# Optimization experiments

Hardware: AMD Instinct MI355X
Metric: run time of the kernel (lower is better)

Reference implementation:

```python
import jax, jax.numpy as jnp
import numpy as np
import math

# Dims chosen per input_specs
B, Q, S, T = 8, 64, 64, 64          # batch, queries, stat (segment) count, tokens per segment
H, DH = 8, 64                        # heads, head dim
NH = H * DH                          # num_hiddens = 512
STAT_K, TOKEN_K = 8, 16
NEG = -1e6


def setup_inputs() -> dict:
    key = jax.random.key(0)
    ks = jax.random.split(key, 11)
    f = lambda k, sh: jax.random.normal(k, sh, dtype=jnp.float32)
    w = lambda k: f(k, (NH, NH)) * 0.05  # Linear weights stored as [in, out]
    return {
        "queries": f(ks[0], (B, Q, NH)),
        "stat_keys": f(ks[1], (B, S, NH)),
        "token_keys": f(ks[2], (B * S, T, NH)),
        "values": f(ks[3], (B * S, T, NH)),
        "stat_valid_lens": jax.random.randint(ks[4], (B,), 1, S + 1, dtype=jnp.int32),
        "Wq_stat": w(ks[5]),
        "Wq_token": w(ks[6]),
        "Wk_stat": w(ks[7]),
        "Wk_token": w(ks[8]),
        "Wv": w(ks[9]),
        "Wo": w(ks[10]),
    }


def reference(queries, stat_keys, token_keys, values, stat_valid_lens,
              Wq_stat, Wq_token, Wk_stat, Wk_token, Wv, Wo):
    scale = 1.0 / math.sqrt(DH)

    def split_heads(x):  # [b, L, H*DH] -> [b, H, L, DH]
        b, L, _ = x.shape
        return x.reshape(b, L, H, DH).transpose(0, 2, 1, 3)

    q_stat = split_heads(queries @ Wq_stat)        # [B,H,Q,DH]
    q_tok = split_heads(queries @ Wq_token)        # [B,H,Q,DH]
    k_stat = split_heads(stat_keys @ Wk_stat)      # [B,H,S,DH]
    # token_keys/values come in as [B*S, T, size]; per-head layout [B,H,S,T,DH]
    k_tok = (token_keys @ Wk_token).reshape(B, S, T, H, DH).transpose(0, 3, 1, 2, 4)
    v = (values @ Wv).reshape(B, S, T, H, DH).transpose(0, 3, 1, 2, 4)

    # --- stat-level scores, valid-length mask, top-k sparsification, softmax ---
    stat_scores = jnp.einsum('bhqd,bhsd->bhqs', q_stat, k_stat) * scale  # [B,H,Q,S]
    valid = jnp.arange(S)[None, None, None, :] < stat_valid_lens[:, None, None, None]
    stat_scores = jnp.where(valid, stat_scores, NEG)
    k1 = min(S - 1, STAT_K)
    _, top_idx = jax.lax.top_k(stat_scores, k1)                           # [B,H,Q,k1]
    keep = jax.nn.one_hot(top_idx, S, dtype=stat_scores.dtype).sum(-2) > 0  # [B,H,Q,S]
    stat_w = jax.nn.softmax(jnp.where(keep, stat_scores, NEG), axis=-1)   # [B,H,Q,S]

    # --- token-level scores. NOTE: the original code computes torch.topk but then
    # overwrites with the LAST k2 positions (token_weights[:, :, -k2:] = ...), so the
    # token top-k result is dead code; we faithfully reproduce the last-k2 masking. ---
    tok_scores = jnp.einsum('bhqd,bhstd->bhsqt', q_tok, k_tok) * scale    # [B,H,S,Q,T]
    k2 = min(T - 1, TOKEN_K)
    last_mask = jnp.arange(T) >= (T - k2)
    tok_w = jax.nn.softmax(jnp.where(last_mask, tok_scores, NEG), axis=-1)
    tok_w = tok_w.transpose(0, 1, 3, 2, 4)                                # [B,H,Q,S,T]

    # --- combine hierarchy and attend over values ---
    comb = stat_w[..., None] * tok_w                                      # [B,H,Q,S,T]
    out = jnp.einsum('bhqst,bhstd->bhqd', comb, v)                        # [B,H,Q,DH]
    out = out.transpose(0, 2, 1, 3).reshape(B, Q, NH)
    return out @ Wo
```

## Files before the change

kernel.cpp:

```cpp
#include <hip/hip_runtime.h>
#include <hip/hip_bf16.h>

#define BB 8
#define QQ 64
#define SS 64
#define TT 64
#define HH 8
#define DH 64
#define NHID 512
#define STAT_K 8
#define TOKEN_K 16

typedef short bf16x8 __attribute__((ext_vector_type(8)));
typedef float f32x4 __attribute__((ext_vector_type(4)));

__device__ inline ushort f2bf_rne(float x) {
    union { float f; unsigned u; } v; v.f = x;
    unsigned r = v.u + 0x7fff + ((v.u >> 16) & 1);
    return (ushort)(r >> 16);
}
__device__ inline float bf2f(ushort h) {
    union { unsigned u; float f; } v; v.u = ((unsigned)h) << 16;
    return v.f;
}

__global__ __launch_bounds__(256) void conv_all(
    const float* w0, const float* w1, const float* w2,
    const float* w3, const float* w4, const float* w5,
    const float* queries, const float* stat_keys,
    ushort* wT, ushort* q_hi, ushort* q_lo, ushort* sk_hi, ushort* sk_lo)
{
    const int z = blockIdx.z;
    if (z < 6) {
        const float* srcs[6] = {w0, w1, w2, w3, w4, w5};
        const float* src = srcs[z];
        ushort* hi = wT + (size_t)z * 524288;
        ushort* lo = hi + 262144;
        __shared__ float t[32][33];
        const int c0 = blockIdx.x * 32, r0 = blockIdx.y * 32;
        const int tx = threadIdx.x & 31, ty = threadIdx.x >> 5;
        #pragma unroll
        for (int i = 0; i < 4; ++i)
            t[ty + 8 * i][tx] = src[(r0 + ty + 8 * i) * 512 + c0 + tx];
        __syncthreads();
        #pragma unroll
        for (int i = 0; i < 4; ++i) {
            float x = t[tx][ty + 8 * i];
            ushort h = f2bf_rne(x);
            int o = (c0 + ty + 8 * i) * 512 + r0 + tx;
            hi[o] = h;
            lo[o] = f2bf_rne(x - bf2f(h));
        }
    } else {
        const float* src = (z == 6) ? queries : stat_keys;
        ushort* hi = (z == 6) ? q_hi : sk_hi;
        ushort* lo = (z == 6) ? q_lo : sk_lo;
        int base = (blockIdx.y * 16 + blockIdx.x) * 1024 + threadIdx.x * 4;
        float4 x = *(const float4*)(src + base);
        ushort4 h, l;
        h.x = f2bf_rne(x.x); l.x = f2bf_rne(x.x - bf2f(h.x));
        h.y = f2bf_rne(x.y); l.y = f2bf_rne(x.y - bf2f(h.y));
        h.z = f2bf_rne(x.z); l.z = f2bf_rne(x.z - bf2f(h.z));
        h.w = f2bf_rne(x.w); l.w = f2bf_rne(x.w - bf2f(h.w));
        *(ushort4*)(hi + base) = h;
        *(ushort4*)(lo + base) = l;
    }
}

__global__ __launch_bounds__(256) void gemm_split3(
    const ushort* __restrict__ q_hi, const ushort* __restrict__ q_lo,
    const ushort* __restrict__ sk_hi, const ushort* __restrict__ sk_lo,
    const ushort* __restrict__ wT,
    float* __restrict__ q_stat, float* __restrict__ k_stat,
    float* __restrict__ q_tokf)
{
    const int z = blockIdx.z;
    const ushort* Ah = (z == 1) ? sk_hi : q_hi;
    const ushort* Al = (z == 1) ? sk_lo : q_lo;
    const ushort* Bh = wT + (size_t)z * 524288;
    const ushort* Bl = Bh + 262144;
    float* C = (z == 0) ? q_stat : (z == 1) ? k_stat : q_tokf;
    const int K = 512, N = 512;

    __shared__ ushort As[2][64][40];
    __shared__ ushort Bs[2][64][40];
    const int tid = threadIdx.x;
    const int row0 = blockIdx.y * 64, col0 = blockIdx.x * 64;
    const int wave = tid >> 6, lane = tid & 63;
    const int wm = wave & 1, wn = wave >> 1;
    const int m16 = lane & 15, quad = lane >> 4;
    const int srow = tid >> 2, schunk = tid & 3;

    f32x4 acc[2][2];
    #pragma unroll
    for (int i = 0; i < 2; ++i)
        #pragma unroll
        for (int j = 0; j < 2; ++j)
            #pragma unroll
            for (int r = 0; r < 4; ++r) acc[i][j][r] = 0.f;

    for (int k0 = 0; k0 < K; k0 += 32) {
        const size_t aoff = (size_t)(row0 + srow) * K + k0 + schunk * 8;
        const size_t boff = (size_t)(col0 + srow) * K + k0 + schunk * 8;
        *(uint4*)&As[0][srow][schunk * 8] = *(const uint4*)(Ah + aoff);
        *(uint4*)&Bs[0][srow][schunk * 8] = *(const uint4*)(Bh + boff);
        *(uint4*)&As[1][srow][schunk * 8] = *(const uint4*)(Al + aoff);
        *(uint4*)&Bs[1][srow][schunk * 8] = *(const uint4*)(Bl + boff);
        __syncthreads();

        bf16x8 af[2], bf[2], afl[2], bfl[2];
        #pragma unroll
        for (int i = 0; i < 2; ++i) {
            af[i]  = *(const bf16x8*)&As[0][wm * 32 + i * 16 + m16][quad * 8];
            bf[i]  = *(const bf16x8*)&Bs[0][wn * 32 + i * 16 + m16][quad * 8];
            afl[i] = *(const bf16x8*)&As[1][wm * 32 + i * 16 + m16][quad * 8];
            bfl[i] = *(const bf16x8*)&Bs[1][wn * 32 + i * 16 + m16][quad * 8];
        }
        #pragma unroll
        for (int i = 0; i < 2; ++i)
            #pragma unroll
            for (int j = 0; j < 2; ++j) {
                acc[i][j] = __builtin_amdgcn_mfma_f32_16x16x32_bf16(af[i], bf[j], acc[i][j], 0, 0, 0);
                acc[i][j] = __builtin_amdgcn_mfma_f32_16x16x32_bf16(af[i], bfl[j], acc[i][j], 0, 0, 0);
                acc[i][j] = __builtin_amdgcn_mfma_f32_16x16x32_bf16(afl[i], bf[j], acc[i][j], 0, 0, 0);
            }
        __syncthreads();
    }

    #pragma unroll
    for (int i = 0; i < 2; ++i)
        #pragma unroll
        for (int j = 0; j < 2; ++j) {
            int r0 = row0 + wm * 32 + i * 16 + quad * 4;
            int c = col0 + wn * 32 + j * 16 + m16;
            #pragma unroll
            for (int reg = 0; reg < 4; ++reg)
                C[(size_t)(r0 + reg) * N + c] = acc[i][j][reg];
        }
}

__global__ __launch_bounds__(256) void gemm_out(
    const ushort* __restrict__ Ah, const ushort* __restrict__ Al,
    const ushort* __restrict__ Bh, const ushort* __restrict__ Bl,
    float* __restrict__ C)
{
    const int K = 512, N = 512;
    __shared__ ushort As[2][64][40];
    __shared__ ushort Bs[2][64][40];
    const int tid = threadIdx.x;
    const int row0 = blockIdx.y * 64, col0 = blockIdx.x * 64;
    const int wave = tid >> 6, lane = tid & 63;
    const int wm = wave & 1, wn = wave >> 1;
    const int m16 = lane & 15, quad = lane >> 4;
    const int srow = tid >> 2, schunk = tid & 3;

    f32x4 acc[2][2];
    #pragma unroll
    for (int i = 0; i < 2; ++i)
        #pragma unroll
        for (int j = 0; j < 2; ++j)
            #pragma unroll
            for (int r = 0; r < 4; ++r) acc[i][j][r] = 0.f;

    for (int k0 = 0; k0 < K; k0 += 32) {
        const size_t aoff = (size_t)(row0 + srow) * K + k0 + schunk * 8;
        const size_t boff = (size_t)(col0 + srow) * K + k0 + schunk * 8;
        *(uint4*)&As[0][srow][schunk * 8] = *(const uint4*)(Ah + aoff);
        *(uint4*)&Bs[0][srow][schunk * 8] = *(const uint4*)(Bh + boff);
        *(uint4*)&As[1][srow][schunk * 8] = *(const uint4*)(Al + aoff);
        *(uint4*)&Bs[1][srow][schunk * 8] = *(const uint4*)(Bl + boff);
        __syncthreads();

        bf16x8 af[2], bf[2], afl[2], bfl[2];
        #pragma unroll
        for (int i = 0; i < 2; ++i) {
            af[i]  = *(const bf16x8*)&As[0][wm * 32 + i * 16 + m16][quad * 8];
            bf[i]  = *(const bf16x8*)&Bs[0][wn * 32 + i * 16 + m16][quad * 8];
            afl[i] = *(const bf16x8*)&As[1][wm * 32 + i * 16 + m16][quad * 8];
            bfl[i] = *(const bf16x8*)&Bs[1][wn * 32 + i * 16 + m16][quad * 8];
        }
        #pragma unroll
        for (int i = 0; i < 2; ++i)
            #pragma unroll
            for (int j = 0; j < 2; ++j) {
                acc[i][j] = __builtin_amdgcn_mfma_f32_16x16x32_bf16(af[i], bf[j], acc[i][j], 0, 0, 0);
                acc[i][j] = __builtin_amdgcn_mfma_f32_16x16x32_bf16(af[i], bfl[j], acc[i][j], 0, 0, 0);
                acc[i][j] = __builtin_amdgcn_mfma_f32_16x16x32_bf16(afl[i], bf[j], acc[i][j], 0, 0, 0);
            }
        __syncthreads();
    }

    #pragma unroll
    for (int i = 0; i < 2; ++i)
        #pragma unroll
        for (int j = 0; j < 2; ++j) {
            int r0 = row0 + wm * 32 + i * 16 + quad * 4;
            int c = col0 + wn * 32 + j * 16 + m16;
            #pragma unroll
            for (int reg = 0; reg < 4; ++reg)
                C[(size_t)(r0 + reg) * N + c] = acc[i][j][reg];
        }
}

__global__ __launch_bounds__(256) void gemm_tok(
    const float* __restrict__ token_keys, const float* __restrict__ values,
    const ushort* __restrict__ wkt_h, const ushort* __restrict__ wv_h,
    ushort* __restrict__ k_tok, ushort* __restrict__ v_proj)
{
    const int z = blockIdx.z;
    const float* A = z ? values : token_keys;
    const ushort* Bh = z ? wv_h : wkt_h;
    ushort* C = z ? v_proj : k_tok;
    const int K = 512, N = 512;

    __shared__ ushort As[64][40];
    __shared__ ushort Bs[256][40];
    const int tid = threadIdx.x;
    const int row0 = blockIdx.y * 64, col0 = blockIdx.x * 256;
    const int wave = tid >> 6, lane = tid & 63;
    const int m16 = lane & 15, quad = lane >> 4;
    const int srow = tid >> 2, schunk = tid & 3;

    const int r = row0 + srow;
    const size_t arow = (size_t)((r >> 4) * 64 + 48 + (r & 15)) * K;

    f32x4 acc[4][4];
    #pragma unroll
    for (int i = 0; i < 4; ++i)
        #pragma unroll
        for (int j = 0; j < 4; ++j)
            #pragma unroll
            for (int rr = 0; rr < 4; ++rr) acc[i][j][rr] = 0.f;

    for (int k0 = 0; k0 < K; k0 += 32) {
        const float* ap = A + arow + k0 + schunk * 8;
        float4 x0 = ((const float4*)ap)[0];
        float4 x1 = ((const float4*)ap)[1];
        ushort4 h0, h1;
        h0.x = f2bf_rne(x0.x); h0.y = f2bf_rne(x0.y);
        h0.z = f2bf_rne(x0.z); h0.w = f2bf_rne(x0.w);
        h1.x = f2bf_rne(x1.x); h1.y = f2bf_rne(x1.y);
        h1.z = f2bf_rne(x1.z); h1.w = f2bf_rne(x1.w);
        *(ushort4*)&As[srow][schunk * 8] = h0;
        *(ushort4*)&As[srow][schunk * 8 + 4] = h1;
        #pragma unroll
        for (int i = 0; i < 4; ++i) {
            int v = tid + i * 256;
            int brow = v >> 2, bchunk = v & 3;
            *(uint4*)&Bs[brow][bchunk * 8] =
                *(const uint4*)(Bh + (size_t)(col0 + brow) * K + k0 + bchunk * 8);
        }
        __syncthreads();

        bf16x8 af[4], bf[4];
        #pragma unroll
        for (int i = 0; i < 4; ++i) {
            af[i] = *(const bf16x8*)&As[i * 16 + m16][quad * 8];
            bf[i] = *(const bf16x8*)&Bs[wave * 64 + i * 16 + m16][quad * 8];
        }
        #pragma unroll
        for (int i = 0; i < 4; ++i)
            #pragma unroll
            for (int j = 0; j < 4; ++j)
                acc[i][j] = __builtin_amdgcn_mfma_f32_16x16x32_bf16(af[i], bf[j], acc[i][j], 0, 0, 0);
        __syncthreads();
    }

    #pragma unroll
    for (int i = 0; i < 4; ++i)
        #pragma unroll
        for (int j = 0; j < 4; ++j) {
            int r0 = row0 + i * 16 + quad * 4;
            int c = col0 + wave * 64 + j * 16 + m16;
            #pragma unroll
            for (int reg = 0; reg < 4; ++reg)
                C[(size_t)(r0 + reg) * N + c] = f2bf_rne(acc[i][j][reg]);
        }
}

__global__ __launch_bounds__(64) void stat_topk(
    const float* __restrict__ q_stat, const float* __restrict__ k_stat,
    const int* __restrict__ valid_lens,
    int* __restrict__ sel_idx, float* __restrict__ sel_w)
{
    const int bid = blockIdx.x;
    const int b = bid >> 9;
    const int hq = bid & 511;
    const int h = hq >> 6;
    const int q = hq & 63;
    const int lane = threadIdx.x;

    __shared__ float sq[64];
    sq[lane] = q_stat[(b * QQ + q) * NHID + h * DH + lane];
    __syncthreads();

    const float4* kr = (const float4*)(k_stat + (b * SS + lane) * NHID + h * DH);
    const float4* sq4 = (const float4*)sq;
    float sc = 0.f;
    #pragma unroll
    for (int i = 0; i < 16; ++i) {
        float4 a = sq4[i], kk = kr[i];
        sc += a.x * kk.x + a.y * kk.y + a.z * kk.z + a.w * kk.w;
    }
    sc *= 0.125f;
    if (lane >= valid_lens[b]) sc = -1e6f;

    float my = sc;
    float mv[STAT_K];
    int   mi[STAT_K];
    #pragma unroll
    for (int j = 0; j < STAT_K; ++j) {
        float v = my;
        int idx = lane;
        #pragma unroll
        for (int off = 32; off > 0; off >>= 1) {
            float ov = __shfl_down(v, off);
            int   oi = __shfl_down(idx, off);
            if (ov > v || (ov == v && oi < idx)) { v = ov; idx = oi; }
        }
        v = __shfl(v, 0);
        idx = __shfl(idx, 0);
        mv[j] = v; mi[j] = idx;
        if (lane == idx) my = -3e38f;
    }
    float m0 = mv[0];
    float den = 0.f;
    float w[STAT_K];
    #pragma unroll
    for (int j = 0; j < STAT_K; ++j) { w[j] = __expf(mv[j] - m0); den += w[j]; }
    float inv = 1.f / den;
    if (lane < STAT_K) {
        sel_idx[bid * STAT_K + lane] = mi[lane];
        sel_w[bid * STAT_K + lane]   = w[lane] * inv;
    }
}

__global__ __launch_bounds__(64) void token_attend2(
    const float* __restrict__ q_tok, const ushort* __restrict__ k_tok,
    const ushort* __restrict__ v_proj, const int* __restrict__ sel_idx,
    const float* __restrict__ sel_w,
    ushort* __restrict__ ctx_hi, ushort* __restrict__ ctx_lo)
{
    const int bid = blockIdx.x;
    const int b = bid >> 9, h = (bid >> 6) & 7, q = bid & 63;
    const int lane = threadIdx.x;

    __shared__ float sq[64];
    __shared__ float ssc[16];
    __shared__ int   ssel[STAT_K];
    __shared__ float ssw[STAT_K];

    sq[lane] = q_tok[(size_t)(b * QQ + q) * NHID + h * DH + lane];
    if (lane < STAT_K) {
        ssel[lane] = sel_idx[bid * STAT_K + lane];
        ssw[lane]  = sel_w[bid * STAT_K + lane];
    }
    __syncthreads();

    const int t = lane >> 2, part = lane & 3;
    float acc = 0.f;

    for (int j = 0; j < STAT_K; ++j) {
        const int s = ssel[j];
        const float wseg = ssw[j];
        const size_t rowbase = (size_t)((b * SS + s) * TOKEN_K);

        const uint4* k4 = (const uint4*)(k_tok + (rowbase + t) * NHID + h * DH + part * 16);
        uint4 ka = k4[0], kb = k4[1];
        const float* qb = &sq[part * 16];
        float p = 0.f;
        p += qb[0]  * bf2f((ushort)(ka.x & 0xffff)) + qb[1]  * bf2f((ushort)(ka.x >> 16));
        p += qb[2]  * bf2f((ushort)(ka.y & 0xffff)) + qb[3]  * bf2f((ushort)(ka.y >> 16));
        p += qb[4]  * bf2f((ushort)(ka.z & 0xffff)) + qb[5]  * bf2f((ushort)(ka.z >> 16));
        p += qb[6]  * bf2f((ushort)(ka.w & 0xffff)) + qb[7]  * bf2f((ushort)(ka.w >> 16));
        p += qb[8]  * bf2f((ushort)(kb.x & 0xffff)) + qb[9]  * bf2f((ushort)(kb.x >> 16));
        p += qb[10] * bf2f((ushort)(kb.y & 0xffff)) + qb[11] * bf2f((ushort)(kb.y >> 16));
        p += qb[12] * bf2f((ushort)(kb.z & 0xffff)) + qb[13] * bf2f((ushort)(kb.z >> 16));
        p += qb[14] * bf2f((ushort)(kb.w & 0xffff)) + qb[15] * bf2f((ushort)(kb.w >> 16));
        p += __shfl_xor(p, 1);
        p += __shfl_xor(p, 2);
        if (part == 0) ssc[t] = p * 0.125f;
        __syncthreads();

        float m = ssc[0];
        #pragma unroll
        for (int tt = 1; tt < TOKEN_K; ++tt) m = fmaxf(m, ssc[tt]);
        float den = 0.f, wv[TOKEN_K];
        #pragma unroll
        for (int tt = 0; tt < TOKEN_K; ++tt) { wv[tt] = __expf(ssc[tt] - m); den += wv[tt]; }

        const ushort* vrow = v_proj + rowbase * NHID + h * DH + lane;
        float loc = 0.f;
        #pragma unroll
        for (int tt = 0; tt < TOKEN_K; ++tt) loc += wv[tt] * bf2f(vrow[tt * NHID]);
        acc += (wseg / den) * loc;
        __syncthreads();
    }

    const size_t o = (size_t)(b * QQ + q) * NHID + h * DH + lane;
    ushort hh = f2bf_rne(acc);
    ctx_hi[o] = hh;
    ctx_lo[o] = f2bf_rne(acc - bf2f(hh));
}

extern "C" void kernel_launch(void* const* d_in, const int* in_sizes, int n_in,
                              void* d_out, int out_size, void* d_ws, size_t ws_size,
                              hipStream_t stream) {
    const float* queries    = (const float*)d_in[0];
    const float* stat_keys  = (const float*)d_in[1];
    const float* token_keys = (const float*)d_in[2];
    const float* values     = (const float*)d_in[3];
    const int*   valid_lens = (const int*)d_in[4];
    const float* Wq_stat    = (const float*)d_in[5];
    const float* Wq_token   = (const float*)d_in[6];
    const float* Wk_stat    = (const float*)d_in[7];
    const float* Wk_token   = (const float*)d_in[8];
    const float* Wv         = (const float*)d_in[9];
    const float* Wo         = (const float*)d_in[10];

    char* w = (char*)d_ws;
    ushort* wT      = (ushort*)(w + 0);
    ushort* q_hi    = (ushort*)(w + 6291456);
    ushort* q_lo    = q_hi + 262144;
    ushort* sk_hi   = (ushort*)(w + 7340032);
    ushort* sk_lo   = sk_hi + 262144;
    float*  q_stat  = (float*)(w + 8388608);
    float*  k_stat  = (float*)(w + 9437184);
    float*  q_tokf  = (float*)(w + 10485760);
    ushort* k_tok   = (ushort*)(w + 11534336);
    ushort* v_projp = (ushort*)(w + 19922944);
    ushort* ctx_hi  = (ushort*)(w + 28311552);
    ushort* ctx_lo  = ctx_hi + 262144;
    float*  sel_w   = (float*)(w + 29360128);
    int*    sel_idx = (int*)(w + 29491200);

    ushort* wkt_h = wT + 3 * 524288;
    ushort* wv_h  = wT + 4 * 524288;
    ushort* wo_h  = wT + 5 * 524288, *wo_l = wo_h + 262144;

    conv_all<<<dim3(16, 16, 8), 256, 0, stream>>>(
        Wq_stat, Wk_stat, Wq_token, Wk_token, Wv, Wo,
        queries, stat_keys, wT, q_hi, q_lo, sk_hi, sk_lo);

    gemm_split3<<<dim3(8, 8, 3), 256, 0, stream>>>(
        q_hi, q_lo, sk_hi, sk_lo, wT, q_stat, k_stat, q_tokf);

    stat_topk<<<4096, 64, 0, stream>>>(q_stat, k_stat, valid_lens, sel_idx, sel_w);

    gemm_tok<<<dim3(2, 128, 2), 256, 0, stream>>>(
        token_keys, values, wkt_h, wv_h, k_tok, v_projp);

    token_attend2<<<4096, 64, 0, stream>>>(q_tokf, k_tok, v_projp,
                                           sel_idx, sel_w, ctx_hi, ctx_lo);

    gemm_out<<<dim3(8, 8), 256, 0, stream>>>(
        ctx_hi, ctx_lo, wo_h, wo_l, (float*)d_out);
}
```

Before: 224.4 us.

## Fuse stat top-k into token attend, convert inputs inside GEMM, register-prefetch tiles

Merges the stat-score top-k kernel into the token attention kernel, so selected indices and weights stay in registers and one launch plus a global round trip are removed. The hi/lo bf16 split of queries and stat keys moves into the projection GEMM's tile load, which drops those workspace buffers and part of the conversion kernel. All three GEMMs now prefetch the next K tile into registers while the current tile is computed. The prefetch raises register pressure, and the fused attention kernel does more serial work per block.

```diff
diff --git a/kernel.cpp b/kernel.cpp
--- a/kernel.cpp
+++ b/kernel.cpp
@@ -24,59 +24,40 @@
     return v.f;
 }
 
-__global__ __launch_bounds__(256) void conv_all(
+__global__ __launch_bounds__(256) void conv_w(
     const float* w0, const float* w1, const float* w2,
-    const float* w3, const float* w4, const float* w5,
-    const float* queries, const float* stat_keys,
-    ushort* wT, ushort* q_hi, ushort* q_lo, ushort* sk_hi, ushort* sk_lo)
+    const float* w3, const float* w4, const float* w5, ushort* wT)
 {
     const int z = blockIdx.z;
-    if (z < 6) {
-        const float* srcs[6] = {w0, w1, w2, w3, w4, w5};
-        const float* src = srcs[z];
-        ushort* hi = wT + (size_t)z * 524288;
-        ushort* lo = hi + 262144;
-        __shared__ float t[32][33];
-        const int c0 = blockIdx.x * 32, r0 = blockIdx.y * 32;
-        const int tx = threadIdx.x & 31, ty = threadIdx.x >> 5;
-        #pragma unroll
-        for (int i = 0; i < 4; ++i)
-            t[ty + 8 * i][tx] = src[(r0 + ty + 8 * i) * 512 + c0 + tx];
-        __syncthreads();
-        #pragma unroll
-        for (int i = 0; i < 4; ++i) {
-            float x = t[tx][ty + 8 * i];
-            ushort h = f2bf_rne(x);
-            int o = (c0 + ty + 8 * i) * 512 + r0 + tx;
-            hi[o] = h;
-            lo[o] = f2bf_rne(x - bf2f(h));
-        }
-    } else {
-        const float* src = (z == 6) ? queries : stat_keys;
-        ushort* hi = (z == 6) ? q_hi : sk_hi;
-        ushort* lo = (z == 6) ? q_lo : sk_lo;
-        int base = (blockIdx.y * 16 + blockIdx.x) * 1024 + threadIdx.x * 4;
-        float4 x = *(const float4*)(src + base);
-        ushort4 h, l;
-        h.x = f2bf_rne(x.x); l.x = f2bf_rne(x.x - bf2f(h.x));
-        h.y = f2bf_rne(x.y); l.y = f2bf_rne(x.y - bf2f(h.y));
-        h.z = f2bf_rne(x.z); l.z = f2bf_rne(x.z - bf2f(h.z));
-        h.w = f2bf_rne(x.w); l.w = f2bf_rne(x.w - bf2f(h.w));
-        *(ushort4*)(hi + base) = h;
-        *(ushort4*)(lo + base) = l;
+    const float* srcs[6] = {w0, w1, w2, w3, w4, w5};
+    const float* src = srcs[z];
+    ushort* hi = wT + (size_t)z * 524288;
+    ushort* lo = hi + 262144;
+    __shared__ float t[32][33];
+    const int c0 = blockIdx.x * 32, r0 = blockIdx.y * 32;
+    const int tx = threadIdx.x & 31, ty = threadIdx.x >> 5;
+    #pragma unroll
+    for (int i = 0; i < 4; ++i)
+        t[ty + 8 * i][tx] = src[(r0 + ty + 8 * i) * 512 + c0 + tx];
+    __syncthreads();
+    #pragma unroll
+    for (int i = 0; i < 4; ++i) {
+        float x = t[tx][ty + 8 * i];
+        ushort h = f2bf_rne(x);
+        int o = (c0 + ty + 8 * i) * 512 + r0 + tx;
+        hi[o] = h;
+        lo[o] = f2bf_rne(x - bf2f(h));
     }
 }
 
 __global__ __launch_bounds__(256) void gemm_split3(
-    const ushort* __restrict__ q_hi, const ushort* __restrict__ q_lo,
-    const ushort* __restrict__ sk_hi, const ushort* __restrict__ sk_lo,
+    const float* __restrict__ queries, const float* __restrict__ stat_keys,
     const ushort* __restrict__ wT,
     float* __restrict__ q_stat, float* __restrict__ k_stat,
     float* __restrict__ q_tokf)
 {
     const int z = blockIdx.z;
-    const ushort* Ah = (z == 1) ? sk_hi : q_hi;
-    const ushort* Al = (z == 1) ? sk_lo : q_lo;
+    const float* Afp = (z == 1) ? stat_keys : queries;
     const ushort* Bh = wT + (size_t)z * 524288;
     const ushort* Bl = Bh + 262144;
     float* C = (z == 0) ? q_stat : (z == 1) ? k_stat : q_tokf;
@@ -91,6 +72,15 @@
     const int m16 = lane & 15, quad = lane >> 4;
     const int srow = tid >> 2, schunk = tid & 3;
 
+    const float*  aptr  = Afp + (size_t)(row0 + srow) * K + schunk * 8;
+    const ushort* bptrh = Bh + (size_t)(col0 + srow) * K + schunk * 8;
+    const ushort* bptrl = Bl + (size_t)(col0 + srow) * K + schunk * 8;
+
+    float4 ax0 = ((const float4*)aptr)[0];
+    float4 ax1 = ((const float4*)aptr)[1];
+    uint4  bvh = *(const uint4*)bptrh;
+    uint4  bvl = *(const uint4*)bptrl;
+
     f32x4 acc[2][2];
     #pragma unroll
     for (int i = 0; i < 2; ++i)
@@ -100,13 +90,29 @@
             for (int r = 0; r < 4; ++r) acc[i][j][r] = 0.f;
 
     for (int k0 = 0; k0 < K; k0 += 32) {
-        const size_t aoff = (size_t)(row0 + srow) * K + k0 + schunk * 8;
-        const size_t boff = (size_t)(col0 + srow) * K + k0 + schunk * 8;
-        *(uint4*)&As[0][srow][schunk * 8] = *(const uint4*)(Ah + aoff);
-        *(uint4*)&Bs[0][srow][schunk * 8] = *(const uint4*)(Bh + boff);
-        *(uint4*)&As[1][srow][schunk * 8] = *(const uint4*)(Al + aoff);
-        *(uint4*)&Bs[1][srow][schunk * 8] = *(const uint4*)(Bl + boff);
-        __syncthreads();
+        ushort4 h0, h1, l0, l1;
+        h0.x = f2bf_rne(ax0.x); l0.x = f2bf_rne(ax0.x - bf2f(h0.x));
+        h0.y = f2bf_rne(ax0.y); l0.y = f2bf_rne(ax0.y - bf2f(h0.y));
+        h0.z = f2bf_rne(ax0.z); l0.z = f2bf_rne(ax0.z - bf2f(h0.z));
+        h0.w = f2bf_rne(ax0.w); l0.w = f2bf_rne(ax0.w - bf2f(h0.w));
+        h1.x = f2bf_rne(ax1.x); l1.x = f2bf_rne(ax1.x - bf2f(h1.x));
+        h1.y = f2bf_rne(ax1.y); l1.y = f2bf_rne(ax1.y - bf2f(h1.y));
+        h1.z = f2bf_rne(ax1.z); l1.z = f2bf_rne(ax1.z - bf2f(h1.z));
+        h1.w = f2bf_rne(ax1.w); l1.w = f2bf_rne(ax1.w - bf2f(h1.w));
+        *(ushort4*)&As[0][srow][schunk * 8]     = h0;
+        *(ushort4*)&As[0][srow][schunk * 8 + 4] = h1;
+        *(ushort4*)&As[1][srow][schunk * 8]     = l0;
+        *(ushort4*)&As[1][srow][schunk * 8 + 4] = l1;
+        *(uint4*)&Bs[0][srow][schunk * 8] = bvh;
+        *(uint4*)&Bs[1][srow][schunk * 8] = bvl;
+        __syncthreads();
+
+        if (k0 + 32 < K) {
+            ax0 = ((const float4*)(aptr + k0 + 32))[0];
+            ax1 = ((const float4*)(aptr + k0 + 32))[1];
+            bvh = *(const uint4*)(bptrh + k0 + 32);
+            bvl = *(const uint4*)(bptrl + k0 + 32);
+        }
 
         bf16x8 af[2], bf[2], afl[2], bfl[2];
         #pragma unroll
@@ -154,6 +160,16 @@
     const int m16 = lane & 15, quad = lane >> 4;
     const int srow = tid >> 2, schunk = tid & 3;
 
+    const ushort* aptrh = Ah + (size_t)(row0 + srow) * K + schunk * 8;
+    const ushort* aptrl = Al + (size_t)(row0 + srow) * K + schunk * 8;
+    const ushort* bptrh = Bh + (size_t)(col0 + srow) * K + schunk * 8;
+    const ushort* bptrl = Bl + (size_t)(col0 + srow) * K + schunk * 8;
+
+    uint4 avh = *(const uint4*)aptrh;
+    uint4 avl = *(const uint4*)aptrl;
+    uint4 bvh = *(const uint4*)bptrh;
+    uint4 bvl = *(const uint4*)bptrl;
+
     f32x4 acc[2][2];
     #pragma unroll
     for (int i = 0; i < 2; ++i)
@@ -163,13 +179,18 @@
             for (int r = 0; r < 4; ++r) acc[i][j][r] = 0.f;
 
     for (int k0 = 0; k0 < K; k0 += 32) {
-        const size_t aoff = (size_t)(row0 + srow) * K + k0 + schunk * 8;
-        const size_t boff = (size_t)(col0 + srow) * K + k0 + schunk * 8;
-        *(uint4*)&As[0][srow][schunk * 8] = *(const uint4*)(Ah + aoff);
-        *(uint4*)&Bs[0][srow][schunk * 8] = *(const uint4*)(Bh + boff);
-        *(uint4*)&As[1][srow][schunk * 8] = *(const uint4*)(Al + aoff);
-        *(uint4*)&Bs[1][srow][schunk * 8] = *(const uint4*)(Bl + boff);
-        __syncthreads();
+        *(uint4*)&As[0][srow][schunk * 8] = avh;
+        *(uint4*)&As[1][srow][schunk * 8] = avl;
+        *(uint4*)&Bs[0][srow][schunk * 8] = bvh;
+        *(uint4*)&Bs[1][srow][schunk * 8] = bvl;
+        __syncthreads();
+
+        if (k0 + 32 < K) {
+            avh = *(const uint4*)(aptrh + k0 + 32);
+            avl = *(const uint4*)(aptrl + k0 + 32);
+            bvh = *(const uint4*)(bptrh + k0 + 32);
+            bvl = *(const uint4*)(bptrl + k0 + 32);
+        }
 
         bf16x8 af[2], bf[2], afl[2], bfl[2];
         #pragma unroll
@@ -222,7 +243,16 @@
     const int srow = tid >> 2, schunk = tid & 3;
 
     const int r = row0 + srow;
-    const size_t arow = (size_t)((r >> 4) * 64 + 48 + (r & 15)) * K;
+    const float* aptr = A + (size_t)((r >> 4) * 64 + 48 + (r & 15)) * K + schunk * 8;
+
+    float4 ax0 = ((const float4*)aptr)[0];
+    float4 ax1 = ((const float4*)aptr)[1];
+    uint4 bv[4];
+    #pragma unroll
+    for (int i = 0; i < 4; ++i) {
+        int v = tid + i * 256;
+        bv[i] = *(const uint4*)(Bh + (size_t)(col0 + (v >> 2)) * K + (v & 3) * 8);
+    }
 
     f32x4 acc[4][4];
     #pragma unroll
@@ -233,24 +263,29 @@
             for (int rr = 0; rr < 4; ++rr) acc[i][j][rr] = 0.f;
 
     for (int k0 = 0; k0 < K; k0 += 32) {
-        const float* ap = A + arow + k0 + schunk * 8;
-        float4 x0 = ((const float4*)ap)[0];
-        float4 x1 = ((const float4*)ap)[1];
         ushort4 h0, h1;
-        h0.x = f2bf_rne(x0.x); h0.y = f2bf_rne(x0.y);
-        h0.z = f2bf_rne(x0.z); h0.w = f2bf_rne(x0.w);
-        h1.x = f2bf_rne(x1.x); h1.y = f2bf_rne(x1.y);
-        h1.z = f2bf_rne(x1.z); h1.w = f2bf_rne(x1.w);
-        *(ushort4*)&As[srow][schunk * 8] = h0;
+        h0.x = f2bf_rne(ax0.x); h0.y = f2bf_rne(ax0.y);
+        h0.z = f2bf_rne(ax0.z); h0.w = f2bf_rne(ax0.w);
+        h1.x = f2bf_rne(ax1.x); h1.y = f2bf_rne(ax1.y);
+        h1.z = f2bf_rne(ax1.z); h1.w = f2bf_rne(ax1.w);
+        *(ushort4*)&As[srow][schunk * 8]     = h0;
         *(ushort4*)&As[srow][schunk * 8 + 4] = h1;
         #pragma unroll
         for (int i = 0; i < 4; ++i) {
             int v = tid + i * 256;
-            int brow = v >> 2, bchunk = v & 3;
-            *(uint4*)&Bs[brow][bchunk * 8] =
-                *(const uint4*)(Bh + (size_t)(col0 + brow) * K + k0 + bchunk * 8);
-        }
-        __syncthreads();
+            *(uint4*)&Bs[v >> 2][(v & 3) * 8] = bv[i];
+        }
+        __syncthreads();
+
+        if (k0 + 32 < K) {
+            ax0 = ((const float4*)(aptr + k0 + 32))[0];
+            ax1 = ((const float4*)(aptr + k0 + 32))[1];
+            #pragma unroll
+            for (int i = 0; i < 4; ++i) {
+                int v = tid + i * 256;
+                bv[i] = *(const uint4*)(Bh + (size_t)(col0 + (v >> 2)) * K + (v & 3) * 8 + k0 + 32);
+            }
+        }
 
         bf16x8 af[4], bf[4];
         #pragma unroll
@@ -278,67 +313,10 @@
         }
 }
 
-__global__ __launch_bounds__(64) void stat_topk(
+__global__ __launch_bounds__(64) void attend_fused(
     const float* __restrict__ q_stat, const float* __restrict__ k_stat,
-    const int* __restrict__ valid_lens,
-    int* __restrict__ sel_idx, float* __restrict__ sel_w)
-{
-    const int bid = blockIdx.x;
-    const int b = bid >> 9;
-    const int hq = bid & 511;
-    const int h = hq >> 6;
-    const int q = hq & 63;
-    const int lane = threadIdx.x;
-
-    __shared__ float sq[64];
-    sq[lane] = q_stat[(b * QQ + q) * NHID + h * DH + lane];
-    __syncthreads();
-
-    const float4* kr = (const float4*)(k_stat + (b * SS + lane) * NHID + h * DH);
-    const float4* sq4 = (const float4*)sq;
-    float sc = 0.f;
-    #pragma unroll
-    for (int i = 0; i < 16; ++i) {
-        float4 a = sq4[i], kk = kr[i];
-        sc += a.x * kk.x + a.y * kk.y + a.z * kk.z + a.w * kk.w;
-    }
-    sc *= 0.125f;
-    if (lane >= valid_lens[b]) sc = -1e6f;
-
-    float my = sc;
-    float mv[STAT_K];
-    int   mi[STAT_K];
-    #pragma unroll
-    for (int j = 0; j < STAT_K; ++j) {
-        float v = my;
-        int idx = lane;
-        #pragma unroll
-        for (int off = 32; off > 0; off >>= 1) {
-            float ov = __shfl_down(v, off);
-            int   oi = __shfl_down(idx, off);
-            if (ov > v || (ov == v && oi < idx)) { v = ov; idx = oi; }
-        }
-        v = __shfl(v, 0);
-        idx = __shfl(idx, 0);
-        mv[j] = v; mi[j] = idx;
-        if (lane == idx) my = -3e38f;
-    }
-    float m0 = mv[0];
-    float den = 0.f;
-    float w[STAT_K];
-    #pragma unroll
-    for (int j = 0; j < STAT_K; ++j) { w[j] = __expf(mv[j] - m0); den += w[j]; }
-    float inv = 1.f / den;
-    if (lane < STAT_K) {
-        sel_idx[bid * STAT_K + lane] = mi[lane];
-        sel_w[bid * STAT_K + lane]   = w[lane] * inv;
-    }
-}
-
-__global__ __launch_bounds__(64) void token_attend2(
     const float* __restrict__ q_tok, const ushort* __restrict__ k_tok,
-    const ushort* __restrict__ v_proj, const int* __restrict__ sel_idx,
-    const float* __restrict__ sel_w,
+    const ushort* __restrict__ v_proj, const int* __restrict__ valid_lens,
     ushort* __restrict__ ctx_hi, ushort* __restrict__ ctx_lo)
 {
     const int bid = blockIdx.x;
@@ -347,60 +325,91 @@
 
     __shared__ float sq[64];
     __shared__ float ssc[16];
-    __shared__ int   ssel[STAT_K];
-    __shared__ float ssw[STAT_K];
-
-    sq[lane] = q_tok[(size_t)(b * QQ + q) * NHID + h * DH + lane];
-    if (lane < STAT_K) {
-        ssel[lane] = sel_idx[bid * STAT_K + lane];
-        ssw[lane]  = sel_w[bid * STAT_K + lane];
-    }
+
+    sq[lane] = q_stat[(b * QQ + q) * NHID + h * DH + lane];
     __syncthreads();
-
-    const int t = lane >> 2, part = lane & 3;
-    float acc = 0.f;
-
-    for (int j = 0; j < STAT_K; ++j) {
-        const int s = ssel[j];
-        const float wseg = ssw[j];
-        const size_t rowbase = (size_t)((b * SS + s) * TOKEN_K);
-
-        const uint4* k4 = (const uint4*)(k_tok + (rowbase + t) * NHID + h * DH + part * 16);
-        uint4 ka = k4[0], kb = k4[1];
-        const float* qb = &sq[part * 16];
-        float p = 0.f;
-        p += qb[0]  * bf2f((ushort)(ka.x & 0xffff)) + qb[1]  * bf2f((ushort)(ka.x >> 16));
-        p += qb[2]  * bf2f((ushort)(ka.y & 0xffff)) + qb[3]  * bf2f((ushort)(ka.y >> 16));
-        p += qb[4]  * bf2f((ushort)(ka.z & 0xffff)) + qb[5]  * bf2f((ushort)(ka.z >> 16));
-        p += qb[6]  * bf2f((ushort)(ka.w & 0xffff)) + qb[7]  * bf2f((ushort)(ka.w >> 16));
-        p += qb[8]  * bf2f((ushort)(kb.x & 0xffff)) + qb[9]  * bf2f((ushort)(kb.x >> 16));
-        p += qb[10] * bf2f((ushort)(kb.y & 0xffff)) + qb[11] * bf2f((ushort)(kb.y >> 16));
-        p += qb[12] * bf2f((ushort)(kb.z & 0xffff)) + qb[13] * bf2f((ushort)(kb.z >> 16));
-        p += qb[14] * bf2f((ushort)(kb.w & 0xffff)) + qb[15] * bf2f((ushort)(kb.w >> 16));
-        p += __shfl_xor(p, 1);
-        p += __shfl_xor(p, 2);
-        if (part == 0) ssc[t] = p * 0.125f;
-        __syncthreads();
-
-        float m = ssc[0];
-        #pragma unroll
-        for (int tt = 1; tt < TOKEN_K; ++tt) m = fmaxf(m, ssc[tt]);
-        float den = 0.f, wv[TOKEN_K];
-        #pragma unroll
-        for (int tt = 0; tt < TOKEN_K; ++tt) { wv[tt] = __expf(ssc[tt] - m); den += wv[tt]; }
-
-        const ushort* vrow = v_proj + rowbase * NHID + h * DH + lane;
-        float loc = 0.f;
-        #pragma unroll
-        for (int tt = 0; tt < TOKEN_K; ++tt) loc += wv[tt] * bf2f(vrow[tt * NHID]);
-        acc += (wseg / den) * loc;
-        __syncthreads();
-    }
-
-    const size_t o = (size_t)(b * QQ + q) * NHID + h * DH + lane;
-    ushort hh = f2bf_rne(acc);
-    ctx_hi[o] = hh;
-    ctx_lo[o] = f2bf_rne(acc - bf2f(hh));
+    {
+        const float4* kr = (const float4*)(k_stat + (b * SS + lane) * NHID + h * DH);
+        const float4* sq4 = (const float4*)sq;
+        float sc = 0.f;
+        #pragma unroll
+        for (int i = 0; i < 16; ++i) {
+            float4 a = sq4[i], kk = kr[i];
+            sc += a.x * kk.x + a.y * kk.y + a.z * kk.z + a.w * kk.w;
+        }
+        sc *= 0.125f;
+        if (lane >= valid_lens[b]) sc = -1e6f;
+
+        float my = sc;
+        float mv[STAT_K]; int mi[STAT_K];
+        #pragma unroll
+        for (int j = 0; j < STAT_K; ++j) {
+            float v = my; int idx = lane;
+            #pragma unroll
+            for (int off = 32; off > 0; off >>= 1) {
+                float ov = __shfl_down(v, off);
+                int   oi = __shfl_down(idx, off);
+                if (ov > v || (ov == v && oi < idx)) { v = ov; idx = oi; }
+            }
+            v = __shfl(v, 0); idx = __shfl(idx, 0);
+            mv[j] = v; mi[j] = idx;
+            if (lane == idx) my = -3e38f;
+        }
+        float m0 = mv[0], den = 0.f, w[STAT_K];
+        #pragma unroll
+        for (int j = 0; j < STAT_K; ++j) { w[j] = __expf(mv[j] - m0); den += w[j]; }
+        float inv = 1.f / den;
+
+        __syncthreads();
+        sq[lane] = q_tok[(size_t)(b * QQ + q) * NHID + h * DH + lane];
+        __syncthreads();
+
+        const int t = lane >> 2, part = lane & 3;
+        float acc = 0.f;
+
+        #pragma unroll
+        for (int j = 0; j < STAT_K; ++j) {
+            const int s = mi[j];
+            const float wseg = w[j] * inv;
+            const size_t rowbase = (size_t)((b * SS + s) * TOKEN_K);
+
+            const uint4* k4 = (const uint4*)(k_tok + (rowbase + t) * NHID + h * DH + part * 16);
+            uint4 ka = k4[0], kb = k4[1];
+            const float* qb = &sq[part * 16];
+            float p = 0.f;
+            p += qb[0]  * bf2f((ushort)(ka.x & 0xffff)) + qb[1]  * bf2f((ushort)(ka.x >> 16));
+            p += qb[2]  * bf2f((ushort)(ka.y & 0xffff)) + qb[3]  * bf2f((ushort)(ka.y >> 16));
+            p += qb[4]  * bf2f((ushort)(ka.z & 0xffff)) + qb[5]  * bf2f((ushort)(ka.z >> 16));
+            p += qb[6]  * bf2f((ushort)(ka.w & 0xffff)) + qb[7]  * bf2f((ushort)(ka.w >> 16));
+            p += qb[8]  * bf2f((ushort)(kb.x & 0xffff)) + qb[9]  * bf2f((ushort)(kb.x >> 16));
+            p += qb[10] * bf2f((ushort)(kb.y & 0xffff)) + qb[11] * bf2f((ushort)(kb.y >> 16));
+            p += qb[12] * bf2f((ushort)(kb.z & 0xffff)) + qb[13] * bf2f((ushort)(kb.z >> 16));
+            p += qb[14] * bf2f((ushort)(kb.w & 0xffff)) + qb[15] * bf2f((ushort)(kb.w >> 16));
+            p += __shfl_xor(p, 1);
+            p += __shfl_xor(p, 2);
+            if (part == 0) ssc[t] = p * 0.125f;
+            __syncthreads();
+
+            float m = ssc[0];
+            #pragma unroll
+            for (int tt = 1; tt < TOKEN_K; ++tt) m = fmaxf(m, ssc[tt]);
+            float dent = 0.f, wv[TOKEN_K];
+            #pragma unroll
+            for (int tt = 0; tt < TOKEN_K; ++tt) { wv[tt] = __expf(ssc[tt] - m); dent += wv[tt]; }
+
+            const ushort* vrow = v_proj + rowbase * NHID + h * DH + lane;
+            float loc = 0.f;
+            #pragma unroll
+            for (int tt = 0; tt < TOKEN_K; ++tt) loc += wv[tt] * bf2f(vrow[tt * NHID]);
+            acc += (wseg / dent) * loc;
+            __syncthreads();
+        }
+
+        const size_t o = (size_t)(b * QQ + q) * NHID + h * DH + lane;
+        ushort hh = f2bf_rne(acc);
+        ctx_hi[o] = hh;
+        ctx_lo[o] = f2bf_rne(acc - bf2f(hh));
+    }
 }
 
 extern "C" void kernel_launch(void* const* d_in, const int* in_sizes, int n_in,
@@ -420,38 +429,29 @@
 
     char* w = (char*)d_ws;
     ushort* wT      = (ushort*)(w + 0);
-    ushort* q_hi    = (ushort*)(w + 6291456);
-    ushort* q_lo    = q_hi + 262144;
-    ushort* sk_hi   = (ushort*)(w + 7340032);
-    ushort* sk_lo   = sk_hi + 262144;
-    float*  q_stat  = (float*)(w + 8388608);
-    float*  k_stat  = (float*)(w + 9437184);
-    float*  q_tokf  = (float*)(w + 10485760);
-    ushort* k_tok   = (ushort*)(w + 11534336);
-    ushort* v_projp = (ushort*)(w + 19922944);
-    ushort* ctx_hi  = (ushort*)(w + 28311552);
+    float*  q_stat  = (float*)(w + 6291456);
+    float*  k_stat  = (float*)(w + 7340032);
+    float*  q_tokf  = (float*)(w + 8388608);
+    ushort* k_tok   = (ushort*)(w + 9437184);
+    ushort* v_projp = (ushort*)(w + 17825792);
+    ushort* ctx_hi  = (ushort*)(w + 26214400);
     ushort* ctx_lo  = ctx_hi + 262144;
-    float*  sel_w   = (float*)(w + 29360128);
-    int*    sel_idx = (int*)(w + 29491200);
 
     ushort* wkt_h = wT + 3 * 524288;
     ushort* wv_h  = wT + 4 * 524288;
     ushort* wo_h  = wT + 5 * 524288, *wo_l = wo_h + 262144;
 
-    conv_all<<<dim3(16, 16, 8), 256, 0, stream>>>(
-        Wq_stat, Wk_stat, Wq_token, Wk_token, Wv, Wo,
-        queries, stat_keys, wT, q_hi, q_lo, sk_hi, sk_lo);
+    conv_w<<<dim3(16, 16, 6), 256, 0, stream>>>(
+        Wq_stat, Wk_stat, Wq_token, Wk_token, Wv, Wo, wT);
 
     gemm_split3<<<dim3(8, 8, 3), 256, 0, stream>>>(
-        q_hi, q_lo, sk_hi, sk_lo, wT, q_stat, k_stat, q_tokf);
-
-    stat_topk<<<4096, 64, 0, stream>>>(q_stat, k_stat, valid_lens, sel_idx, sel_w);
+        queries, stat_keys, wT, q_stat, k_stat, q_tokf);
 
     gemm_tok<<<dim3(2, 128, 2), 256, 0, stream>>>(
         token_keys, values, wkt_h, wv_h, k_tok, v_projp);
 
-    token_attend2<<<4096, 64, 0, stream>>>(q_tokf, k_tok, v_projp,
-                                           sel_idx, sel_w, ctx_hi, ctx_lo);
+    attend_fused<<<4096, 64, 0, stream>>>(
+        q_stat, k_stat, q_tokf, k_tok, v_projp, valid_lens, ctx_hi, ctx_lo);
 
     gemm_out<<<dim3(8, 8), 256, 0, stream>>>(
         ctx_hi, ctx_lo, wo_h, wo_l, (float*)d_out);
```

Measured after the change: 269.6 us. +20.1%, slower.
